# Kernel tuning notes

Hardware: AMD Instinct MI355X
Metric: run time of the kernel (lower is better)

Reference implementation:

```python
import jax, jax.numpy as jnp
import numpy as np

V, BLK, C, H, L = 50257, 1024, 1024, 16, 4
B, T = 2, 1024
D = C // H
EPS = 1e-5

def _ln(x, w):
    mu = jnp.mean(x, axis=-1, keepdims=True)
    var = jnp.mean(jnp.square(x - mu), axis=-1, keepdims=True)
    return (x - mu) * jax.lax.rsqrt(var + EPS) * w

def setup_inputs() -> dict:
    key = jax.random.key(0)
    ks = jax.random.split(key, 9)
    s = 0.02
    return {
        'idx': jax.random.randint(ks[0], (B, T), 0, V),
        'wte': jax.random.normal(ks[1], (V, C), jnp.float32) * s,
        'wpe': jax.random.normal(ks[2], (BLK, C), jnp.float32) * s,
        'ln1_w': jnp.ones((L, C), jnp.float32),
        'attn_w': jax.random.normal(ks[3], (L, 3 * C, C), jnp.float32) * s,   # torch Linear [out,in]
        'attnproj_w': jax.random.normal(ks[4], (L, C, C), jnp.float32) * (s / np.sqrt(2 * L)),
        'ln2_w': jnp.ones((L, C), jnp.float32),
        'fc_w': jax.random.normal(ks[5], (L, 4 * C, C), jnp.float32) * s,
        'mlpproj_w': jax.random.normal(ks[6], (L, C, 4 * C), jnp.float32) * (s / np.sqrt(2 * L)),
        'lnf_w': jnp.ones((C,), jnp.float32),
        'head_w': jax.random.normal(ks[7], (V, C), jnp.float32) * s,
    }

def _block(x, ln1_w, attn_w, attnproj_w, ln2_w, fc_w, mlpproj_w):
    b, t, c = x.shape
    h = _ln(x, ln1_w)
    qkv = h @ attn_w.T                                  # [B,T,3C]
    q, k, v = jnp.split(qkv, 3, axis=-1)
    q = q.reshape(b, t, H, D).transpose(0, 2, 1, 3)      # [B,H,T,D]
    k = k.reshape(b, t, H, D).transpose(0, 2, 1, 3)
    v = v.reshape(b, t, H, D).transpose(0, 2, 1, 3)
    att = jnp.einsum('bhqd,bhkd->bhqk', q, k) * (1.0 / np.sqrt(D))
    causal = jnp.tril(jnp.ones((t, t), bool))
    att = jnp.where(causal, att, jnp.float32(-jnp.inf))
    p = jax.nn.softmax(att, axis=-1)
    y = jnp.einsum('bhqk,bhkd->bhqd', p, v)
    y = y.transpose(0, 2, 1, 3).reshape(b, t, c)
    y = y @ attnproj_w.T
    x = x + y
    m = _ln(x, ln2_w)
    m = jax.nn.relu(m @ fc_w.T) @ mlpproj_w.T
    return x + m

def reference(idx, wte, wpe, ln1_w, attn_w, attnproj_w, ln2_w, fc_w, mlpproj_w, lnf_w, head_w):
    t = idx.shape[1]
    x = wte[idx] + wpe[:t]                               # [B,T,C]
    for i in range(L):
        x = _block(x, ln1_w[i], attn_w[i], attnproj_w[i], ln2_w[i], fc_w[i], mlpproj_w[i])
    x = _ln(x, lnf_w)
    return x @ head_w.T                                  # logits [B,T,V]
```

## Files before the change

kernel.cpp:

```cpp
#include <hip/hip_runtime.h>

typedef __bf16 bf16x8 __attribute__((ext_vector_type(8)));
typedef float f32x4 __attribute__((ext_vector_type(4)));
typedef unsigned short u16x8 __attribute__((ext_vector_type(8)));

#define LOG2E 1.4426950408889634f

__device__ __forceinline__ unsigned short f2bf(float f) {
  union { float f; unsigned u; } v; v.f = f;
  return (unsigned short)((v.u + 0x7fffu + ((v.u >> 16) & 1u)) >> 16);
}

__device__ __forceinline__ void gload16(const void* g, void* l) {
  __builtin_amdgcn_global_load_lds(
      (const __attribute__((address_space(1))) unsigned int*)g,
      (__attribute__((address_space(3))) unsigned int*)l, 16, 0, 0);
}

__global__ __launch_bounds__(256) void cvt_kernel(
    const float* __restrict__ s, unsigned short* __restrict__ d, int n8) {
  int i = blockIdx.x * 256 + threadIdx.x;
  int stride = gridDim.x * 256;
  for (; i < n8; i += stride) {
    float4 a = ((const float4*)s)[2 * i];
    float4 b = ((const float4*)s)[2 * i + 1];
    u16x8 o;
    o[0] = f2bf(a.x); o[1] = f2bf(a.y); o[2] = f2bf(a.z); o[3] = f2bf(a.w);
    o[4] = f2bf(b.x); o[5] = f2bf(b.y); o[6] = f2bf(b.z); o[7] = f2bf(b.w);
    ((u16x8*)d)[i] = o;
  }
}

__global__ __launch_bounds__(256) void embed_kernel(
    const int* __restrict__ idx, const float* __restrict__ wte,
    const float* __restrict__ wpe, float* __restrict__ x) {
  int row = blockIdx.x;
  int tok = idx[row];
  int t = row & 1023;
  float4 a = ((const float4*)(wte + (size_t)tok * 1024))[threadIdx.x];
  float4 p = ((const float4*)(wpe + (size_t)t * 1024))[threadIdx.x];
  a.x += p.x; a.y += p.y; a.z += p.z; a.w += p.w;
  ((float4*)(x + (size_t)row * 1024))[threadIdx.x] = a;
}

__global__ __launch_bounds__(256) void ln_kernel(
    const float* __restrict__ x, const float* __restrict__ w,
    unsigned short* __restrict__ out) {
  __shared__ float2 red[4];
  int row = blockIdx.x, tid = threadIdx.x;
  float4 v = ((const float4*)(x + (size_t)row * 1024))[tid];
  float s  = v.x + v.y + v.z + v.w;
  float s2 = v.x * v.x + v.y * v.y + v.z * v.z + v.w * v.w;
#pragma unroll
  for (int m = 32; m >= 1; m >>= 1) {
    s  += __shfl_xor(s, m, 64);
    s2 += __shfl_xor(s2, m, 64);
  }
  if ((tid & 63) == 0) red[tid >> 6] = make_float2(s, s2);
  __syncthreads();
  float S = 0.f, S2 = 0.f;
#pragma unroll
  for (int i = 0; i < 4; ++i) { S += red[i].x; S2 += red[i].y; }
  float mu = S * (1.f / 1024.f);
  float var = S2 * (1.f / 1024.f) - mu * mu;
  float rs = rsqrtf(var + 1e-5f);
  float4 wv = ((const float4*)w)[tid];
  ushort4 o;
  o.x = f2bf((v.x - mu) * rs * wv.x);
  o.y = f2bf((v.y - mu) * rs * wv.y);
  o.z = f2bf((v.z - mu) * rs * wv.z);
  o.w = f2bf((v.w - mu) * rs * wv.w);
  ((ushort4*)(out + (size_t)row * 1024))[tid] = o;
}

template <int MODE, bool WB16>
__global__ __launch_bounds__(256, 2) void gemm_bt(
    const unsigned short* __restrict__ A, const void* __restrict__ Wp,
    void* __restrict__ outp, const float* __restrict__ resid,
    unsigned short* __restrict__ qo, unsigned short* __restrict__ ko,
    unsigned short* __restrict__ vo, int M, int N, int K) {
  __shared__ unsigned short As[2][128 * 64];
  __shared__ unsigned short Bs[2][128 * 64];

  const int tid = threadIdx.x;
  const int lane = tid & 63;
  const int wv = tid >> 6;
  const int lr = lane & 15, lh = lane >> 4;
  const int nbm = M >> 7;
  const int nb = gridDim.x;
  const int bid = blockIdx.x;
  const int swz = (bid & 7) * (nb >> 3) + (bid >> 3);
  const int m0 = (swz % nbm) << 7;
  const int n0 = (swz / nbm) << 7;
  const int wm = (wv >> 1) << 6;
  const int wn = (wv & 1) << 6;
  const int nK = K >> 6;

  float4 breg[8];
  const float* Wf = (const float*)Wp;
  const unsigned short* Wb = (const unsigned short*)Wp;

  auto loadB = [&](int kt) {
#pragma unroll
    for (int j = 0; j < 8; ++j) {
      int u = j * 256 + tid;
      int rn = n0 + (u >> 4);
      if (rn >= N) rn = N - 1;
      breg[j] = *(const float4*)(Wf + (size_t)rn * K + kt * 64 + (u & 15) * 4);
    }
  };
  auto writeB = [&](int buf) {
#pragma unroll
    for (int j = 0; j < 8; ++j) {
      int u = j * 256 + tid;
      int row = u >> 4, q = u & 15;
      ushort4 h4;
      h4.x = f2bf(breg[j].x); h4.y = f2bf(breg[j].y);
      h4.z = f2bf(breg[j].z); h4.w = f2bf(breg[j].w);
      int off = row * 128 + ((q * 8) ^ ((row & 7) << 4));
      *(ushort4*)((char*)(&Bs[buf][0]) + off) = h4;
    }
  };
  auto stageA = [&](int buf, int kt) {
    const unsigned short* base = A + (size_t)m0 * K + kt * 64;
#pragma unroll
    for (int j = 0; j < 4; ++j) {
      int u = j * 256 + tid;
      int row = u >> 3, un = u & 7;
      gload16(base + (size_t)row * K + ((un ^ (row & 7)) << 3),
              (char*)(&As[buf][0]) + u * 16);
    }
  };
  auto stageB16 = [&](int buf, int kt) {
#pragma unroll
    for (int j = 0; j < 4; ++j) {
      int u = j * 256 + tid;
      int row = u >> 3, un = u & 7;
      size_t grow = (size_t)(n0 + row);
      if constexpr (MODE == 4) { if ((int)grow >= N) grow = N - 1; }
      gload16(Wb + grow * K + kt * 64 + ((un ^ (row & 7)) << 3),
              (char*)(&Bs[buf][0]) + u * 16);
    }
  };

  f32x4 acc[4][4];
#pragma unroll
  for (int a = 0; a < 4; ++a)
#pragma unroll
    for (int b = 0; b < 4; ++b) acc[a][b] = f32x4{0.f, 0.f, 0.f, 0.f};

  if constexpr (WB16) {
    stageA(0, 0);
    stageB16(0, 0);
  } else {
    loadB(0);
    stageA(0, 0);
    writeB(0);
  }
  __syncthreads();

  for (int kt = 0; kt < nK; ++kt) {
    int cur = kt & 1;
    if constexpr (WB16) {
      if (kt + 1 < nK) { stageA(cur ^ 1, kt + 1); stageB16(cur ^ 1, kt + 1); }
    } else {
      if (kt + 1 < nK) { loadB(kt + 1); stageA(cur ^ 1, kt + 1); }
    }

    bf16x8 af[4][2], bf[4][2];
#pragma unroll
    for (int mi = 0; mi < 4; ++mi)
#pragma unroll
      for (int ks = 0; ks < 2; ++ks) {
        int row = wm + mi * 16 + lr;
        int off = row * 128 + ((ks * 64 + lh * 16) ^ ((row & 7) << 4));
        af[mi][ks] = *(const bf16x8*)((const char*)(&As[cur][0]) + off);
      }
#pragma unroll
    for (int ni = 0; ni < 4; ++ni)
#pragma unroll
      for (int ks = 0; ks < 2; ++ks) {
        int row = wn + ni * 16 + lr;
        int off = row * 128 + ((ks * 64 + lh * 16) ^ ((row & 7) << 4));
        bf[ni][ks] = *(const bf16x8*)((const char*)(&Bs[cur][0]) + off);
      }
#pragma unroll
    for (int ks = 0; ks < 2; ++ks)
#pragma unroll
      for (int mi = 0; mi < 4; ++mi)
#pragma unroll
        for (int ni = 0; ni < 4; ++ni)
          acc[mi][ni] = __builtin_amdgcn_mfma_f32_16x16x32_bf16(
              af[mi][ks], bf[ni][ks], acc[mi][ni], 0, 0, 0);

    if constexpr (!WB16) {
      if (kt + 1 < nK) writeB(cur ^ 1);
    }
    __syncthreads();
  }

#pragma unroll
  for (int mi = 0; mi < 4; ++mi)
#pragma unroll
    for (int ni = 0; ni < 4; ++ni)
#pragma unroll
      for (int r = 0; r < 4; ++r) {
        int grow = m0 + wm + mi * 16 + lh * 4 + r;
        int gcol = n0 + wn + ni * 16 + lr;
        float val = acc[mi][ni][r];
        if constexpr (MODE == 1) val = fmaxf(val, 0.f);
        if constexpr (MODE == 0 || MODE == 1) {
          ((unsigned short*)outp)[(size_t)grow * N + gcol] = f2bf(val);
        } else if constexpr (MODE == 2) {
          ((float*)outp)[(size_t)grow * N + gcol] =
              resid[(size_t)grow * N + gcol] + val;
        } else if constexpr (MODE == 3) {
          int which = gcol >> 10, hh = (gcol >> 6) & 15, dd = gcol & 63;
          int b = grow >> 10, t = grow & 1023;
          unsigned short hv = f2bf(val);
          size_t bh = (size_t)(b * 16 + hh) << 16;
          if (which == 0)      qo[bh + t * 64 + dd] = hv;
          else if (which == 1) ko[bh + t * 64 + dd] = hv;
          else                 vo[bh + dd * 1024 + t] = hv;
        } else {
          if (gcol < N)
            ((float*)outp)[(size_t)grow * (size_t)N + gcol] = val;
        }
      }
}

template <int MODE>
__global__ __launch_bounds__(256, 2) void gemm128_bt(
    const unsigned short* __restrict__ A, const unsigned short* __restrict__ Wb,
    void* __restrict__ outp, const float* __restrict__ resid,
    unsigned short* __restrict__ qo, unsigned short* __restrict__ ko,
    unsigned short* __restrict__ vo, int M, int N, int K) {
  __shared__ unsigned short As[4][128 * 32];
  __shared__ unsigned short Bs[4][128 * 32];

  const int tid = threadIdx.x;
  const int lane = tid & 63;
  const int wv = tid >> 6;
  const int lr = lane & 15, lh = lane >> 4;
  const int nbm = M >> 7;
  const int nb = gridDim.x;
  const int bid = blockIdx.x;
  const int swz = (bid & 7) * (nb >> 3) + (bid >> 3);
  const int m0 = (swz % nbm) << 7;
  const int n0 = (swz / nbm) << 7;
  const int wm = (wv >> 1) << 6;
  const int wn = (wv & 1) << 6;
  const int nK = K >> 5;

  size_t aoff[2], boff[2];
  int ldst[2];
#pragma unroll
  for (int j = 0; j < 2; ++j) {
    int u = j * 256 + tid;
    int p = u >> 3, s = u & 7;
    int ss = s ^ (p & 7);
    int arow = m0 + 2 * p + (ss >> 2);
    int brow = n0 + 2 * p + (ss >> 2);
    if (brow >= N) brow = N - 1;
    aoff[j] = (size_t)arow * K + (ss & 3) * 8;
    boff[j] = (size_t)brow * K + (ss & 3) * 8;
    ldst[j] = u * 16;
  }

  auto stage = [&](int buf, int k) {
#pragma unroll
    for (int j = 0; j < 2; ++j)
      gload16(A + aoff[j] + k * 32, (char*)(&As[buf][0]) + ldst[j]);
#pragma unroll
    for (int j = 0; j < 2; ++j)
      gload16(Wb + boff[j] + k * 32, (char*)(&Bs[buf][0]) + ldst[j]);
  };

  f32x4 acc[4][4];
#pragma unroll
  for (int a = 0; a < 4; ++a)
#pragma unroll
    for (int b = 0; b < 4; ++b) acc[a][b] = f32x4{0.f, 0.f, 0.f, 0.f};

  stage(0, 0);
  if (nK > 1) stage(1, 1);
  if (nK > 2) stage(2, 2);
  if (nK > 2)      asm volatile("s_waitcnt vmcnt(8)" ::: "memory");
  else if (nK > 1) asm volatile("s_waitcnt vmcnt(4)" ::: "memory");
  else             asm volatile("s_waitcnt vmcnt(0)" ::: "memory");
  __builtin_amdgcn_s_barrier();
  __builtin_amdgcn_sched_barrier(0);

  for (int kt = 0; kt < nK; ++kt) {
    const int buf = kt & 3;
    bf16x8 af[4], bfr[4];
#pragma unroll
    for (int ni = 0; ni < 4; ++ni) {
      int r = wn + ni * 16 + lr;
      int p = r >> 1;
      int off = p * 128 + (((((r & 1) << 2) | lh) ^ (p & 7)) << 4);
      bfr[ni] = *(const bf16x8*)((const char*)(&Bs[buf][0]) + off);
    }
#pragma unroll
    for (int mi = 0; mi < 4; ++mi) {
      int r = wm + mi * 16 + lr;
      int p = r >> 1;
      int off = p * 128 + (((((r & 1) << 2) | lh) ^ (p & 7)) << 4);
      af[mi] = *(const bf16x8*)((const char*)(&As[buf][0]) + off);
    }
    if (kt + 3 < nK) stage((kt + 3) & 3, kt + 3);

    __builtin_amdgcn_s_setprio(1);
#pragma unroll
    for (int mi = 0; mi < 4; ++mi)
#pragma unroll
      for (int ni = 0; ni < 4; ++ni)
        acc[mi][ni] = __builtin_amdgcn_mfma_f32_16x16x32_bf16(
            af[mi], bfr[ni], acc[mi][ni], 0, 0, 0);
    __builtin_amdgcn_s_setprio(0);

    if (kt + 1 < nK) {
      if (kt + 4 <= nK)      asm volatile("s_waitcnt vmcnt(8)" ::: "memory");
      else if (kt + 3 <= nK) asm volatile("s_waitcnt vmcnt(4)" ::: "memory");
      else                   asm volatile("s_waitcnt vmcnt(0)" ::: "memory");
      __builtin_amdgcn_s_barrier();
      __builtin_amdgcn_sched_barrier(0);
    }
  }

#pragma unroll
  for (int mi = 0; mi < 4; ++mi)
#pragma unroll
    for (int ni = 0; ni < 4; ++ni)
#pragma unroll
      for (int r = 0; r < 4; ++r) {
        int grow = m0 + wm + mi * 16 + lh * 4 + r;
        int gcol = n0 + wn + ni * 16 + lr;
        float val = acc[mi][ni][r];
        if constexpr (MODE == 1) val = fmaxf(val, 0.f);
        if constexpr (MODE == 0 || MODE == 1) {
          ((unsigned short*)outp)[(size_t)grow * N + gcol] = f2bf(val);
        } else if constexpr (MODE == 2) {
          ((float*)outp)[(size_t)grow * N + gcol] =
              resid[(size_t)grow * N + gcol] + val;
        } else if constexpr (MODE == 3) {
          int which = gcol >> 10, hh = (gcol >> 6) & 15, dd = gcol & 63;
          int b = grow >> 10, t = grow & 1023;
          unsigned short hv = f2bf(val);
          size_t bh = (size_t)(b * 16 + hh) << 16;
          if (which == 0)      qo[bh + t * 64 + dd] = hv;
          else if (which == 1) ko[bh + t * 64 + dd] = hv;
          else                 vo[bh + dd * 1024 + t] = hv;
        } else {
          if (gcol < N)
            ((float*)outp)[(size_t)grow * (size_t)N + gcol] = val;
        }
      }
}

__global__ __launch_bounds__(512, 2) void gemm256_bt(
    const unsigned short* __restrict__ A, const unsigned short* __restrict__ Wb,
    float* __restrict__ out, int M, int N, int K) {
  __shared__ unsigned short As[4][256 * 32];
  __shared__ unsigned short Bs[4][256 * 32];

  const int tid = threadIdx.x;
  const int lane = tid & 63;
  const int wv = tid >> 6;
  const int lr = lane & 15, lh = lane >> 4;
  const int wm = (wv >> 2) * 128;
  const int wn = (wv & 3) * 64;
  const int nbm = M >> 8;
  const int nb = gridDim.x;
  const int bid = blockIdx.x;
  const int swz = (bid & 7) * (nb >> 3) + (bid >> 3);
  const int m0 = (swz % nbm) << 8;
  const int n0 = (swz / nbm) << 8;
  const int nK = K >> 5;

  size_t aoff[2], boff[2];
  int ldst[2];
#pragma unroll
  for (int j = 0; j < 2; ++j) {
    int u = j * 512 + tid;
    int p = u >> 3, s = u & 7;
    int ss = s ^ (p & 7);
    int arow = m0 + 2 * p + (ss >> 2);
    int brow = n0 + 2 * p + (ss >> 2);
    if (brow >= N) brow = N - 1;
    aoff[j] = (size_t)arow * K + (ss & 3) * 8;
    boff[j] = (size_t)brow * K + (ss & 3) * 8;
    ldst[j] = u * 16;
  }

  auto stage = [&](int buf, int k) {
#pragma unroll
    for (int j = 0; j < 2; ++j)
      gload16(A + aoff[j] + k * 32, (char*)(&As[buf][0]) + ldst[j]);
#pragma unroll
    for (int j = 0; j < 2; ++j)
      gload16(Wb + boff[j] + k * 32, (char*)(&Bs[buf][0]) + ldst[j]);
  };

  f32x4 acc[8][4];
#pragma unroll
  for (int a = 0; a < 8; ++a)
#pragma unroll
    for (int b = 0; b < 4; ++b) acc[a][b] = f32x4{0.f, 0.f, 0.f, 0.f};

  stage(0, 0);
  if (nK > 1) stage(1, 1);
  if (nK > 2) stage(2, 2);
  if (nK > 2) asm volatile("s_waitcnt vmcnt(8)" ::: "memory");
  else        asm volatile("s_waitcnt vmcnt(0)" ::: "memory");
  __builtin_amdgcn_s_barrier();
  __builtin_amdgcn_sched_barrier(0);

  for (int k = 0; k < nK; ++k) {
    const int buf = k & 3;
    bf16x8 af[8], bfr[4];
#pragma unroll
    for (int ni = 0; ni < 4; ++ni) {
      int r = wn + ni * 16 + lr;
      int p = r >> 1;
      int off = p * 128 + (((((r & 1) << 2) | lh) ^ (p & 7)) << 4);
      bfr[ni] = *(const bf16x8*)((const char*)(&Bs[buf][0]) + off);
    }
#pragma unroll
    for (int mi = 0; mi < 8; ++mi) {
      int r = wm + mi * 16 + lr;
      int p = r >> 1;
      int off = p * 128 + (((((r & 1) << 2) | lh) ^ (p & 7)) << 4);
      af[mi] = *(const bf16x8*)((const char*)(&As[buf][0]) + off);
    }
    if (k + 3 < nK) stage((k + 3) & 3, k + 3);

    __builtin_amdgcn_s_setprio(1);
#pragma unroll
    for (int mi = 0; mi < 8; ++mi)
#pragma unroll
      for (int ni = 0; ni < 4; ++ni)
        acc[mi][ni] = __builtin_amdgcn_mfma_f32_16x16x32_bf16(
            af[mi], bfr[ni], acc[mi][ni], 0, 0, 0);
    __builtin_amdgcn_s_setprio(0);

    if (k + 1 < nK) {
      if (k + 4 <= nK)      asm volatile("s_waitcnt vmcnt(8)" ::: "memory");
      else if (k + 3 <= nK) asm volatile("s_waitcnt vmcnt(4)" ::: "memory");
      else                  asm volatile("s_waitcnt vmcnt(0)" ::: "memory");
      __builtin_amdgcn_s_barrier();
      __builtin_amdgcn_sched_barrier(0);
    }
  }

#pragma unroll
  for (int mi = 0; mi < 8; ++mi)
#pragma unroll
    for (int ni = 0; ni < 4; ++ni)
#pragma unroll
      for (int r = 0; r < 4; ++r) {
        int grow = m0 + wm + mi * 16 + lh * 4 + r;
        int gcol = n0 + wn + ni * 16 + lr;
        if (gcol < N) out[(size_t)grow * (size_t)N + gcol] = acc[mi][ni][r];
      }
}

__global__ __launch_bounds__(256, 2) void attn_kernel(
    const unsigned short* __restrict__ qb, const unsigned short* __restrict__ kb,
    const unsigned short* __restrict__ vt, unsigned short* __restrict__ yb) {
  __shared__ unsigned short Ks[2][64 * 64];
  __shared__ unsigned short Vs[2][64 * 64];
  __shared__ unsigned short Ps[4][32 * 64];

  const int tid = threadIdx.x, lane = tid & 63, wv = tid >> 6;
  const int lr = lane & 15, lh = lane >> 4;
  const int bid = blockIdx.x;
  const int bh = bid >> 3, qt = bid & 7;
  const int q0 = qt << 7;
  const unsigned short* qp = qb + ((size_t)bh << 16);
  const unsigned short* kp = kb + ((size_t)bh << 16);
  const unsigned short* vp = vt + ((size_t)bh << 16);

  bf16x8 qf[2][2];
#pragma unroll
  for (int mi = 0; mi < 2; ++mi)
#pragma unroll
    for (int ks = 0; ks < 2; ++ks) {
      int row = q0 + wv * 32 + mi * 16 + lr;
      qf[mi][ks] = *(const bf16x8*)(qp + (size_t)row * 64 + ks * 32 + lh * 8);
    }

  f32x4 o[2][4];
  float mr[2][4], lsum[2][4];
#pragma unroll
  for (int mi = 0; mi < 2; ++mi) {
#pragma unroll
    for (int di = 0; di < 4; ++di) o[mi][di] = f32x4{0.f, 0.f, 0.f, 0.f};
#pragma unroll
    for (int r = 0; r < 4; ++r) { mr[mi][r] = -1e30f; lsum[mi][r] = 0.f; }
  }

  const int wqmax = q0 + wv * 32 + 31;
  const int ntiles = (q0 + 128) >> 6;

  auto stageKV = [&](int buf, int t) {
    int kv0 = t << 6;
#pragma unroll
    for (int j = 0; j < 2; ++j) {
      int u = j * 256 + tid;
      int row = u >> 3, un = u & 7;
      gload16(kp + (size_t)(kv0 + row) * 64 + ((un ^ (row & 7)) << 3),
              (char*)(&Ks[buf][0]) + u * 16);
      gload16(vp + (size_t)row * 1024 + kv0 + ((un ^ (row & 7)) << 3),
              (char*)(&Vs[buf][0]) + u * 16);
    }
  };

  stageKV(0, 0);

  for (int t = 0; t < ntiles; ++t) {
    __syncthreads();
    if (t + 1 < ntiles) stageKV((t + 1) & 1, t + 1);
    int cur = t & 1;
    int kv0 = t << 6;
    if (kv0 <= wqmax) {
      f32x4 s[2][4];
#pragma unroll
      for (int mi = 0; mi < 2; ++mi)
#pragma unroll
        for (int ni = 0; ni < 4; ++ni) s[mi][ni] = f32x4{0.f, 0.f, 0.f, 0.f};

      bf16x8 kf[4][2];
#pragma unroll
      for (int ni = 0; ni < 4; ++ni)
#pragma unroll
        for (int ks = 0; ks < 2; ++ks) {
          int row = ni * 16 + lr;
          int off = row * 128 + ((ks * 64 + lh * 16) ^ ((row & 7) << 4));
          kf[ni][ks] = *(const bf16x8*)((const char*)(&Ks[cur][0]) + off);
        }
#pragma unroll
      for (int ks = 0; ks < 2; ++ks)
#pragma unroll
        for (int mi = 0; mi < 2; ++mi)
#pragma unroll
          for (int ni = 0; ni < 4; ++ni)
            s[mi][ni] = __builtin_amdgcn_mfma_f32_16x16x32_bf16(
                qf[mi][ks], kf[ni][ks], s[mi][ni], 0, 0, 0);

#pragma unroll
      for (int mi = 0; mi < 2; ++mi)
#pragma unroll
        for (int r = 0; r < 4; ++r) {
          int rowq = q0 + wv * 32 + mi * 16 + lh * 4 + r;
          float xv[4];
          float pm = -1e30f;
#pragma unroll
          for (int ni = 0; ni < 4; ++ni) {
            int col = kv0 + ni * 16 + lr;
            float xx = s[mi][ni][r] * 0.125f;
            if (col > rowq) xx = -1e30f;
            xv[ni] = xx;
            pm = fmaxf(pm, xx);
          }
#pragma unroll
          for (int msk = 1; msk < 16; msk <<= 1)
            pm = fmaxf(pm, __shfl_xor(pm, msk, 64));
          float mnew = fmaxf(mr[mi][r], pm);
          float al = exp2f((mr[mi][r] - mnew) * LOG2E);
          mr[mi][r] = mnew;
          float ps = 0.f;
#pragma unroll
          for (int ni = 0; ni < 4; ++ni) {
            float p = exp2f((xv[ni] - mnew) * LOG2E);
            s[mi][ni][r] = p;
            ps += p;
          }
#pragma unroll
          for (int msk = 1; msk < 16; msk <<= 1) ps += __shfl_xor(ps, msk, 64);
          lsum[mi][r] = lsum[mi][r] * al + ps;
#pragma unroll
          for (int di = 0; di < 4; ++di) o[mi][di][r] *= al;
        }

#pragma unroll
      for (int mi = 0; mi < 2; ++mi)
#pragma unroll
        for (int ni = 0; ni < 4; ++ni)
#pragma unroll
          for (int r = 0; r < 4; ++r) {
            int row = mi * 16 + lh * 4 + r;
            int off = row * 128 + (((ni * 16 + lr) * 2) ^ ((row & 7) << 4));
            *(unsigned short*)((char*)(&Ps[wv][0]) + off) = f2bf(s[mi][ni][r]);
          }

      bf16x8 pf[2][2], vf[4][2];
#pragma unroll
      for (int mi = 0; mi < 2; ++mi)
#pragma unroll
        for (int ks = 0; ks < 2; ++ks) {
          int row = mi * 16 + lr;
          int off = row * 128 + ((ks * 64 + lh * 16) ^ ((row & 7) << 4));
          pf[mi][ks] = *(const bf16x8*)((const char*)(&Ps[wv][0]) + off);
        }
#pragma unroll
      for (int di = 0; di < 4; ++di)
#pragma unroll
        for (int ks = 0; ks < 2; ++ks) {
          int row = di * 16 + lr;
          int off = row * 128 + ((ks * 64 + lh * 16) ^ ((row & 7) << 4));
          vf[di][ks] = *(const bf16x8*)((const char*)(&Vs[cur][0]) + off);
        }
#pragma unroll
      for (int ks = 0; ks < 2; ++ks)
#pragma unroll
        for (int mi = 0; mi < 2; ++mi)
#pragma unroll
          for (int di = 0; di < 4; ++di)
            o[mi][di] = __builtin_amdgcn_mfma_f32_16x16x32_bf16(
                pf[mi][ks], vf[di][ks], o[mi][di], 0, 0, 0);
    }
  }

  int b = bh >> 4, hh = bh & 15;
#pragma unroll
  for (int mi = 0; mi < 2; ++mi)
#pragma unroll
    for (int r = 0; r < 4; ++r) {
      float inv = 1.f / lsum[mi][r];
      int rowq = q0 + wv * 32 + mi * 16 + lh * 4 + r;
      size_t mg = (size_t)(b * 1024 + rowq) * 1024 + hh * 64;
#pragma unroll
      for (int di = 0; di < 4; ++di)
        yb[mg + di * 16 + lr] = f2bf(o[mi][di][r] * inv);
    }
}

extern "C" void kernel_launch(void* const* d_in, const int* in_sizes, int n_in,
                              void* d_out, int out_size, void* d_ws,
                              size_t ws_size, hipStream_t stream) {
  const int*   idx  = (const int*)d_in[0];
  const float* wte  = (const float*)d_in[1];
  const float* wpe  = (const float*)d_in[2];
  const float* ln1w = (const float*)d_in[3];
  const float* attnw= (const float*)d_in[4];
  const float* aprj = (const float*)d_in[5];
  const float* ln2w = (const float*)d_in[6];
  const float* fcw  = (const float*)d_in[7];
  const float* mprj = (const float*)d_in[8];
  const float* lnfw = (const float*)d_in[9];
  const float* hw   = (const float*)d_in[10];
  float* out = (float*)d_out;
  char* ws = (char*)d_ws;

  float* x            = (float*)ws;
  unsigned short* h   = (unsigned short*)(ws + ((size_t)8 << 20));
  unsigned short* qbf = (unsigned short*)(ws + ((size_t)12 << 20));
  unsigned short* kbf = (unsigned short*)(ws + ((size_t)16 << 20));
  unsigned short* vtb = (unsigned short*)(ws + ((size_t)20 << 20));
  unsigned short* ybf = (unsigned short*)(ws + ((size_t)24 << 20));
  unsigned short* mhb = (unsigned short*)(ws + ((size_t)12 << 20));

  size_t off = (size_t)28 << 20;
  unsigned short* attnw16 = (unsigned short*)(ws + off); off += (size_t)4 * 3072 * 1024 * 2;
  unsigned short* aprj16  = (unsigned short*)(ws + off); off += (size_t)4 * 1024 * 1024 * 2;
  unsigned short* fcw16   = (unsigned short*)(ws + off); off += (size_t)4 * 4096 * 1024 * 2;
  unsigned short* mprj16  = (unsigned short*)(ws + off); off += (size_t)4 * 1024 * 4096 * 2;
  unsigned short* hw16    = (unsigned short*)(ws + off); off += (size_t)50257 * 1024 * 2;
  const bool b16 = ws_size >= off;

  embed_kernel<<<2048, 256, 0, stream>>>(idx, wte, wpe, x);

  if (b16) {
    cvt_kernel<<<2048, 256, 0, stream>>>(attnw, attnw16, 4 * 3072 * 1024 / 8);
    cvt_kernel<<<2048, 256, 0, stream>>>(aprj,  aprj16,  4 * 1024 * 1024 / 8);
    cvt_kernel<<<2048, 256, 0, stream>>>(fcw,   fcw16,   4 * 4096 * 1024 / 8);
    cvt_kernel<<<2048, 256, 0, stream>>>(mprj,  mprj16,  4 * 1024 * 4096 / 8);
    cvt_kernel<<<2048, 256, 0, stream>>>(hw,    hw16,    50257 * 1024 / 8);
  }

  for (int l = 0; l < 4; ++l) {
    ln_kernel<<<2048, 256, 0, stream>>>(x, ln1w + l * 1024, h);
    if (b16)
      gemm128_bt<3><<<16 * 24, 256, 0, stream>>>(
          h, attnw16 + (size_t)l * 3072 * 1024, nullptr, nullptr, qbf, kbf,
          vtb, 2048, 3072, 1024);
    else
      gemm_bt<3, false><<<16 * 24, 256, 0, stream>>>(
          h, attnw + (size_t)l * 3072 * 1024, nullptr, nullptr, qbf, kbf, vtb,
          2048, 3072, 1024);
    attn_kernel<<<256, 256, 0, stream>>>(qbf, kbf, vtb, ybf);
    if (b16)
      gemm128_bt<2><<<16 * 8, 256, 0, stream>>>(
          ybf, aprj16 + (size_t)l * 1024 * 1024, x, x, nullptr, nullptr,
          nullptr, 2048, 1024, 1024);
    else
      gemm_bt<2, false><<<16 * 8, 256, 0, stream>>>(
          ybf, aprj + (size_t)l * 1024 * 1024, x, x, nullptr, nullptr, nullptr,
          2048, 1024, 1024);
    ln_kernel<<<2048, 256, 0, stream>>>(x, ln2w + l * 1024, h);
    if (b16)
      gemm128_bt<1><<<16 * 32, 256, 0, stream>>>(
          h, fcw16 + (size_t)l * 4096 * 1024, mhb, nullptr, nullptr, nullptr,
          nullptr, 2048, 4096, 1024);
    else
      gemm_bt<1, false><<<16 * 32, 256, 0, stream>>>(
          h, fcw + (size_t)l * 4096 * 1024, mhb, nullptr, nullptr, nullptr,
          nullptr, 2048, 4096, 1024);
    if (b16)
      gemm128_bt<2><<<16 * 8, 256, 0, stream>>>(
          mhb, mprj16 + (size_t)l * 1024 * 4096, x, x, nullptr, nullptr,
          nullptr, 2048, 1024, 4096);
    else
      gemm_bt<2, false><<<16 * 8, 256, 0, stream>>>(
          mhb, mprj + (size_t)l * 1024 * 4096, x, x, nullptr, nullptr, nullptr,
          2048, 1024, 4096);
  }

  ln_kernel<<<2048, 256, 0, stream>>>(x, lnfw, h);
  if (b16)
    gemm256_bt<<<8 * 197, 512, 0, stream>>>(h, hw16, out, 2048, 50257, 1024);
  else
    gemm_bt<4, false><<<16 * 393, 256, 0, stream>>>(
        h, hw, out, nullptr, nullptr, nullptr, nullptr, 2048, 50257, 1024);
}
```

Measured before the change: 1.317 ms.

## Balance causal attention work and use 128x64 GEMM tiles for N=1024 projections

The attention kernel now pairs query strip j with strip 15-j in each block, so every block does a roughly equal share of causal KV tiles and the tail of long blocks disappears. A new gemm64n_bt kernel with 128x64 output tiles replaces the 128x128 tile for the two N=1024 projection GEMMs. This doubles the grid from 128 to 256 blocks so more CUs are busy. The cost is lower per-block data reuse and some predicated MFMA branching in attention.

```diff
diff --git a/kernel.cpp b/kernel.cpp
--- a/kernel.cpp
+++ b/kernel.cpp
@@ -358,6 +358,139 @@
       }
 }
 
+template <int MODE>
+__global__ __launch_bounds__(256, 2) void gemm64n_bt(
+    const unsigned short* __restrict__ A, const unsigned short* __restrict__ Wb,
+    void* __restrict__ outp, const float* __restrict__ resid,
+    unsigned short* __restrict__ qo, unsigned short* __restrict__ ko,
+    unsigned short* __restrict__ vo, int M, int N, int K) {
+  __shared__ unsigned short As[4][128 * 32];
+  __shared__ unsigned short Bs[4][64 * 32];
+
+  const int tid = threadIdx.x;
+  const int lane = tid & 63;
+  const int wv = tid >> 6;
+  const int lr = lane & 15, lh = lane >> 4;
+  const int nbm = M >> 7;
+  const int nb = gridDim.x;
+  const int bid = blockIdx.x;
+  const int swz = (bid & 7) * (nb >> 3) + (bid >> 3);
+  const int m0 = (swz % nbm) << 7;
+  const int n0 = (swz / nbm) << 6;
+  const int wm = (wv >> 1) << 6;
+  const int wn = (wv & 1) << 5;
+  const int nK = K >> 5;
+
+  size_t aoff[2], boff;
+  int ldsta[2], ldstb;
+#pragma unroll
+  for (int j = 0; j < 2; ++j) {
+    int u = j * 256 + tid;
+    int p = u >> 3, s = u & 7;
+    int ss = s ^ (p & 7);
+    int arow = m0 + 2 * p + (ss >> 2);
+    aoff[j] = (size_t)arow * K + (ss & 3) * 8;
+    ldsta[j] = u * 16;
+  }
+  {
+    int u = tid;
+    int p = u >> 3, s = u & 7;
+    int ss = s ^ (p & 7);
+    int brow = n0 + 2 * p + (ss >> 2);
+    if (brow >= N) brow = N - 1;
+    boff = (size_t)brow * K + (ss & 3) * 8;
+    ldstb = u * 16;
+  }
+
+  auto stage = [&](int buf, int k) {
+#pragma unroll
+    for (int j = 0; j < 2; ++j)
+      gload16(A + aoff[j] + k * 32, (char*)(&As[buf][0]) + ldsta[j]);
+    gload16(Wb + boff + k * 32, (char*)(&Bs[buf][0]) + ldstb);
+  };
+
+  f32x4 acc[4][2];
+#pragma unroll
+  for (int a = 0; a < 4; ++a)
+#pragma unroll
+    for (int b = 0; b < 2; ++b) acc[a][b] = f32x4{0.f, 0.f, 0.f, 0.f};
+
+  stage(0, 0);
+  if (nK > 1) stage(1, 1);
+  if (nK > 2) stage(2, 2);
+  if (nK > 2)      asm volatile("s_waitcnt vmcnt(6)" ::: "memory");
+  else if (nK > 1) asm volatile("s_waitcnt vmcnt(3)" ::: "memory");
+  else             asm volatile("s_waitcnt vmcnt(0)" ::: "memory");
+  __builtin_amdgcn_s_barrier();
+  __builtin_amdgcn_sched_barrier(0);
+
+  for (int kt = 0; kt < nK; ++kt) {
+    const int buf = kt & 3;
+    bf16x8 af[4], bfr[2];
+#pragma unroll
+    for (int ni = 0; ni < 2; ++ni) {
+      int r = wn + ni * 16 + lr;
+      int p = r >> 1;
+      int off = p * 128 + (((((r & 1) << 2) | lh) ^ (p & 7)) << 4);
+      bfr[ni] = *(const bf16x8*)((const char*)(&Bs[buf][0]) + off);
+    }
+#pragma unroll
+    for (int mi = 0; mi < 4; ++mi) {
+      int r = wm + mi * 16 + lr;
+      int p = r >> 1;
+      int off = p * 128 + (((((r & 1) << 2) | lh) ^ (p & 7)) << 4);
+      af[mi] = *(const bf16x8*)((const char*)(&As[buf][0]) + off);
+    }
+    if (kt + 3 < nK) stage((kt + 3) & 3, kt + 3);
+
+    __builtin_amdgcn_s_setprio(1);
+#pragma unroll
+    for (int mi = 0; mi < 4; ++mi)
+#pragma unroll
+      for (int ni = 0; ni < 2; ++ni)
+        acc[mi][ni] = __builtin_amdgcn_mfma_f32_16x16x32_bf16(
+            af[mi], bfr[ni], acc[mi][ni], 0, 0, 0);
+    __builtin_amdgcn_s_setprio(0);
+
+    if (kt + 1 < nK) {
+      if (kt + 4 <= nK)      asm volatile("s_waitcnt vmcnt(6)" ::: "memory");
+      else if (kt + 3 <= nK) asm volatile("s_waitcnt vmcnt(3)" ::: "memory");
+      else                   asm volatile("s_waitcnt vmcnt(0)" ::: "memory");
+      __builtin_amdgcn_s_barrier();
+      __builtin_amdgcn_sched_barrier(0);
+    }
+  }
+
+#pragma unroll
+  for (int mi = 0; mi < 4; ++mi)
+#pragma unroll
+    for (int ni = 0; ni < 2; ++ni)
+#pragma unroll
+      for (int r = 0; r < 4; ++r) {
+        int grow = m0 + wm + mi * 16 + lh * 4 + r;
+        int gcol = n0 + wn + ni * 16 + lr;
+        float val = acc[mi][ni][r];
+        if constexpr (MODE == 1) val = fmaxf(val, 0.f);
+        if constexpr (MODE == 0 || MODE == 1) {
+          ((unsigned short*)outp)[(size_t)grow * N + gcol] = f2bf(val);
+        } else if constexpr (MODE == 2) {
+          ((float*)outp)[(size_t)grow * N + gcol] =
+              resid[(size_t)grow * N + gcol] + val;
+        } else if constexpr (MODE == 3) {
+          int which = gcol >> 10, hh = (gcol >> 6) & 15, dd = gcol & 63;
+          int b = grow >> 10, t = grow & 1023;
+          unsigned short hv = f2bf(val);
+          size_t bh = (size_t)(b * 16 + hh) << 16;
+          if (which == 0)      qo[bh + t * 64 + dd] = hv;
+          else if (which == 1) ko[bh + t * 64 + dd] = hv;
+          else                 vo[bh + dd * 1024 + t] = hv;
+        } else {
+          if (gcol < N)
+            ((float*)outp)[(size_t)grow * (size_t)N + gcol] = val;
+        }
+      }
+}
+
 __global__ __launch_bounds__(512, 2) void gemm256_bt(
     const unsigned short* __restrict__ A, const unsigned short* __restrict__ Wb,
     float* __restrict__ out, int M, int N, int K) {
@@ -475,8 +608,9 @@
   const int tid = threadIdx.x, lane = tid & 63, wv = tid >> 6;
   const int lr = lane & 15, lh = lane >> 4;
   const int bid = blockIdx.x;
-  const int bh = bid >> 3, qt = bid & 7;
-  const int q0 = qt << 7;
+  const int bh = bid & 31, j = bid >> 5;
+  const int rb0 = j * 64 + wv * 16;
+  const int rb1 = (15 - j) * 64 + wv * 16;
   const unsigned short* qp = qb + ((size_t)bh << 16);
   const unsigned short* kp = kb + ((size_t)bh << 16);
   const unsigned short* vp = vt + ((size_t)bh << 16);
@@ -486,7 +620,7 @@
   for (int mi = 0; mi < 2; ++mi)
 #pragma unroll
     for (int ks = 0; ks < 2; ++ks) {
-      int row = q0 + wv * 32 + mi * 16 + lr;
+      int row = (mi ? rb1 : rb0) + lr;
       qf[mi][ks] = *(const bf16x8*)(qp + (size_t)row * 64 + ks * 32 + lh * 8);
     }
 
@@ -500,14 +634,13 @@
     for (int r = 0; r < 4; ++r) { mr[mi][r] = -1e30f; lsum[mi][r] = 0.f; }
   }
 
-  const int wqmax = q0 + wv * 32 + 31;
-  const int ntiles = (q0 + 128) >> 6;
+  const int ntiles = 16 - j;
 
   auto stageKV = [&](int buf, int t) {
     int kv0 = t << 6;
 #pragma unroll
-    for (int j = 0; j < 2; ++j) {
-      int u = j * 256 + tid;
+    for (int jj = 0; jj < 2; ++jj) {
+      int u = jj * 256 + tid;
       int row = u >> 3, un = u & 7;
       gload16(kp + (size_t)(kv0 + row) * 64 + ((un ^ (row & 7)) << 3),
               (char*)(&Ks[buf][0]) + u * 16);
@@ -523,103 +656,114 @@
     if (t + 1 < ntiles) stageKV((t + 1) & 1, t + 1);
     int cur = t & 1;
     int kv0 = t << 6;
-    if (kv0 <= wqmax) {
-      f32x4 s[2][4];
-#pragma unroll
-      for (int mi = 0; mi < 2; ++mi)
-#pragma unroll
-        for (int ni = 0; ni < 4; ++ni) s[mi][ni] = f32x4{0.f, 0.f, 0.f, 0.f};
-
-      bf16x8 kf[4][2];
+    const bool act0 = (t <= j);
+
+    f32x4 s[2][4];
+#pragma unroll
+    for (int mi = 0; mi < 2; ++mi)
+#pragma unroll
+      for (int ni = 0; ni < 4; ++ni) s[mi][ni] = f32x4{0.f, 0.f, 0.f, 0.f};
+
+    bf16x8 kf[4][2];
+#pragma unroll
+    for (int ni = 0; ni < 4; ++ni)
+#pragma unroll
+      for (int ks = 0; ks < 2; ++ks) {
+        int row = ni * 16 + lr;
+        int off = row * 128 + ((ks * 64 + lh * 16) ^ ((row & 7) << 4));
+        kf[ni][ks] = *(const bf16x8*)((const char*)(&Ks[cur][0]) + off);
+      }
+#pragma unroll
+    for (int ks = 0; ks < 2; ++ks)
+#pragma unroll
+      for (int ni = 0; ni < 4; ++ni) {
+        if (act0)
+          s[0][ni] = __builtin_amdgcn_mfma_f32_16x16x32_bf16(
+              qf[0][ks], kf[ni][ks], s[0][ni], 0, 0, 0);
+        s[1][ni] = __builtin_amdgcn_mfma_f32_16x16x32_bf16(
+            qf[1][ks], kf[ni][ks], s[1][ni], 0, 0, 0);
+      }
+
+#pragma unroll
+    for (int mi = 0; mi < 2; ++mi) {
+      if (mi == 0 && !act0) continue;
+      const int rb = mi ? rb1 : rb0;
+#pragma unroll
+      for (int r = 0; r < 4; ++r) {
+        int rowq = rb + lh * 4 + r;
+        float xv[4];
+        float pm = -1e30f;
+#pragma unroll
+        for (int ni = 0; ni < 4; ++ni) {
+          int col = kv0 + ni * 16 + lr;
+          float xx = s[mi][ni][r] * 0.125f;
+          if (col > rowq) xx = -1e30f;
+          xv[ni] = xx;
+          pm = fmaxf(pm, xx);
+        }
+#pragma unroll
+        for (int msk = 1; msk < 16; msk <<= 1)
+          pm = fmaxf(pm, __shfl_xor(pm, msk, 64));
+        float mnew = fmaxf(mr[mi][r], pm);
+        float al = exp2f((mr[mi][r] - mnew) * LOG2E);
+        mr[mi][r] = mnew;
+        float ps = 0.f;
+#pragma unroll
+        for (int ni = 0; ni < 4; ++ni) {
+          float p = exp2f((xv[ni] - mnew) * LOG2E);
+          s[mi][ni][r] = p;
+          ps += p;
+        }
+#pragma unroll
+        for (int msk = 1; msk < 16; msk <<= 1) ps += __shfl_xor(ps, msk, 64);
+        lsum[mi][r] = lsum[mi][r] * al + ps;
+#pragma unroll
+        for (int di = 0; di < 4; ++di) o[mi][di][r] *= al;
+      }
+    }
+
+#pragma unroll
+    for (int mi = 0; mi < 2; ++mi) {
+      if (mi == 0 && !act0) continue;
 #pragma unroll
       for (int ni = 0; ni < 4; ++ni)
 #pragma unroll
-        for (int ks = 0; ks < 2; ++ks) {
-          int row = ni * 16 + lr;
-          int off = row * 128 + ((ks * 64 + lh * 16) ^ ((row & 7) << 4));
-          kf[ni][ks] = *(const bf16x8*)((const char*)(&Ks[cur][0]) + off);
+        for (int r = 0; r < 4; ++r) {
+          int row = mi * 16 + lh * 4 + r;
+          int off = row * 128 + (((ni * 16 + lr) * 2) ^ ((row & 7) << 4));
+          *(unsigned short*)((char*)(&Ps[wv][0]) + off) = f2bf(s[mi][ni][r]);
         }
-#pragma unroll
-      for (int ks = 0; ks < 2; ++ks)
-#pragma unroll
-        for (int mi = 0; mi < 2; ++mi)
-#pragma unroll
-          for (int ni = 0; ni < 4; ++ni)
-            s[mi][ni] = __builtin_amdgcn_mfma_f32_16x16x32_bf16(
-                qf[mi][ks], kf[ni][ks], s[mi][ni], 0, 0, 0);
-
-#pragma unroll
-      for (int mi = 0; mi < 2; ++mi)
-#pragma unroll
-        for (int r = 0; r < 4; ++r) {
-          int rowq = q0 + wv * 32 + mi * 16 + lh * 4 + r;
-          float xv[4];
-          float pm = -1e30f;
-#pragma unroll
-          for (int ni = 0; ni < 4; ++ni) {
-            int col = kv0 + ni * 16 + lr;
-            float xx = s[mi][ni][r] * 0.125f;
-            if (col > rowq) xx = -1e30f;
-            xv[ni] = xx;
-            pm = fmaxf(pm, xx);
-          }
-#pragma unroll
-          for (int msk = 1; msk < 16; msk <<= 1)
-            pm = fmaxf(pm, __shfl_xor(pm, msk, 64));
-          float mnew = fmaxf(mr[mi][r], pm);
-          float al = exp2f((mr[mi][r] - mnew) * LOG2E);
-          mr[mi][r] = mnew;
-          float ps = 0.f;
-#pragma unroll
-          for (int ni = 0; ni < 4; ++ni) {
-            float p = exp2f((xv[ni] - mnew) * LOG2E);
-            s[mi][ni][r] = p;
-            ps += p;
-          }
-#pragma unroll
-          for (int msk = 1; msk < 16; msk <<= 1) ps += __shfl_xor(ps, msk, 64);
-          lsum[mi][r] = lsum[mi][r] * al + ps;
-#pragma unroll
-          for (int di = 0; di < 4; ++di) o[mi][di][r] *= al;
-        }
-
-#pragma unroll
-      for (int mi = 0; mi < 2; ++mi)
-#pragma unroll
-        for (int ni = 0; ni < 4; ++ni)
-#pragma unroll
-          for (int r = 0; r < 4; ++r) {
-            int row = mi * 16 + lh * 4 + r;
-            int off = row * 128 + (((ni * 16 + lr) * 2) ^ ((row & 7) << 4));
-            *(unsigned short*)((char*)(&Ps[wv][0]) + off) = f2bf(s[mi][ni][r]);
-          }
-
-      bf16x8 pf[2][2], vf[4][2];
-#pragma unroll
-      for (int mi = 0; mi < 2; ++mi)
-#pragma unroll
-        for (int ks = 0; ks < 2; ++ks) {
-          int row = mi * 16 + lr;
-          int off = row * 128 + ((ks * 64 + lh * 16) ^ ((row & 7) << 4));
-          pf[mi][ks] = *(const bf16x8*)((const char*)(&Ps[wv][0]) + off);
-        }
-#pragma unroll
-      for (int di = 0; di < 4; ++di)
-#pragma unroll
-        for (int ks = 0; ks < 2; ++ks) {
-          int row = di * 16 + lr;
-          int off = row * 128 + ((ks * 64 + lh * 16) ^ ((row & 7) << 4));
-          vf[di][ks] = *(const bf16x8*)((const char*)(&Vs[cur][0]) + off);
-        }
-#pragma unroll
-      for (int ks = 0; ks < 2; ++ks)
-#pragma unroll
-        for (int mi = 0; mi < 2; ++mi)
-#pragma unroll
-          for (int di = 0; di < 4; ++di)
-            o[mi][di] = __builtin_amdgcn_mfma_f32_16x16x32_bf16(
-                pf[mi][ks], vf[di][ks], o[mi][di], 0, 0, 0);
-    }
+    }
+
+    bf16x8 pf[2][2], vf[4][2];
+#pragma unroll
+    for (int mi = 0; mi < 2; ++mi) {
+      if (mi == 0 && !act0) continue;
+#pragma unroll
+      for (int ks = 0; ks < 2; ++ks) {
+        int row = mi * 16 + lr;
+        int off = row * 128 + ((ks * 64 + lh * 16) ^ ((row & 7) << 4));
+        pf[mi][ks] = *(const bf16x8*)((const char*)(&Ps[wv][0]) + off);
+      }
+    }
+#pragma unroll
+    for (int di = 0; di < 4; ++di)
+#pragma unroll
+      for (int ks = 0; ks < 2; ++ks) {
+        int row = di * 16 + lr;
+        int off = row * 128 + ((ks * 64 + lh * 16) ^ ((row & 7) << 4));
+        vf[di][ks] = *(const bf16x8*)((const char*)(&Vs[cur][0]) + off);
+      }
+#pragma unroll
+    for (int ks = 0; ks < 2; ++ks)
+#pragma unroll
+      for (int di = 0; di < 4; ++di) {
+        if (act0)
+          o[0][di] = __builtin_amdgcn_mfma_f32_16x16x32_bf16(
+              pf[0][ks], vf[di][ks], o[0][di], 0, 0, 0);
+        o[1][di] = __builtin_amdgcn_mfma_f32_16x16x32_bf16(
+            pf[1][ks], vf[di][ks], o[1][di], 0, 0, 0);
+      }
   }
 
   int b = bh >> 4, hh = bh & 15;
@@ -628,7 +772,7 @@
 #pragma unroll
     for (int r = 0; r < 4; ++r) {
       float inv = 1.f / lsum[mi][r];
-      int rowq = q0 + wv * 32 + mi * 16 + lh * 4 + r;
+      int rowq = (mi ? rb1 : rb0) + lh * 4 + r;
       size_t mg = (size_t)(b * 1024 + rowq) * 1024 + hh * 64;
 #pragma unroll
       for (int di = 0; di < 4; ++di)
@@ -691,7 +835,7 @@
           2048, 3072, 1024);
     attn_kernel<<<256, 256, 0, stream>>>(qbf, kbf, vtb, ybf);
     if (b16)
-      gemm128_bt<2><<<16 * 8, 256, 0, stream>>>(
+      gemm64n_bt<2><<<16 * 16, 256, 0, stream>>>(
           ybf, aprj16 + (size_t)l * 1024 * 1024, x, x, nullptr, nullptr,
           nullptr, 2048, 1024, 1024);
     else
@@ -708,7 +852,7 @@
           h, fcw + (size_t)l * 4096 * 1024, mhb, nullptr, nullptr, nullptr,
           nullptr, 2048, 4096, 1024);
     if (b16)
-      gemm128_bt<2><<<16 * 8, 256, 0, stream>>>(
+      gemm64n_bt<2><<<16 * 16, 256, 0, stream>>>(
           mhb, mprj16 + (size_t)l * 1024 * 4096, x, x, nullptr, nullptr,
           nullptr, 2048, 1024, 4096);
     else
```

After: 1.218 ms. 1.08x faster.
